# Performance work log

Measured on AMD Instinct MI355X. Metric: run time of the kernel, lower is better.

Reference implementation:

```python
import jax, jax.numpy as jnp
import numpy as np

DIM = 768
HEADS = 12
HD = DIM // HEADS  # 64
BASE = 100.0


def rope_sincos(H, W):
    # DINOv3 RopePositionEmbedding: normalize_coords='separate', base=100.0
    dd = HD // 4
    periods = BASE ** (jnp.arange(dd, dtype=jnp.float32) / dd)          # [dd]
    ch = (jnp.arange(H, dtype=jnp.float32) + 0.5) / H                    # pixel centers
    cw = (jnp.arange(W, dtype=jnp.float32) + 0.5) / W
    cy, cx = jnp.meshgrid(ch, cw, indexing='ij')
    coords = 2.0 * jnp.stack([cy, cx], axis=-1).reshape(H * W, 2) - 1.0  # [N,2] in [-1,1]
    angles = 2.0 * jnp.pi * coords[:, :, None] / periods[None, None, :]  # [N,2,dd]
    angles = angles.reshape(H * W, 2 * dd)                               # [N, HD//2]
    angles = jnp.concatenate([angles, angles], axis=-1)                  # [N, HD]
    return jnp.sin(angles), jnp.cos(angles)


def rotate_half(t):
    t1, t2 = jnp.split(t, 2, axis=-1)
    return jnp.concatenate([-t2, t1], axis=-1)


def setup_inputs() -> dict:
    key = jax.random.key(0)
    k1, k2, k3 = jax.random.split(key, 3)
    B, H, W = 2, 48, 48
    x = jax.random.normal(k1, (B, H, W, DIM), dtype=jnp.float32)
    w_qkv = jax.random.normal(k2, (3 * DIM, DIM), dtype=jnp.float32) * 0.02
    b_qkv = jnp.zeros((3 * DIM,), dtype=jnp.float32)
    w_proj = jax.random.normal(k3, (DIM, DIM), dtype=jnp.float32) * 0.02
    b_proj = jnp.zeros((DIM,), dtype=jnp.float32)
    return {"x": x, "w_qkv": w_qkv, "b_qkv": b_qkv, "w_proj": w_proj, "b_proj": b_proj}


def reference(x, w_qkv, b_qkv, w_proj, b_proj):
    B, H, W, C = x.shape
    N = H * W
    xf = x.reshape(B, N, C)
    qkv = xf @ w_qkv.T + b_qkv                                   # [B,N,3C]
    qkv = qkv.reshape(B, N, 3, HEADS, HD).transpose(2, 0, 3, 1, 4)
    q, k, v = qkv[0], qkv[1], qkv[2]                              # [B,h,N,d]
    sin, cos = rope_sincos(H, W)                                  # [N,d]
    q = q * cos + rotate_half(q) * sin
    k = k * cos + rotate_half(k) * sin
    scale = HD ** -0.5
    attn = jax.nn.softmax(jnp.einsum('bhqd,bhkd->bhqk', q, k) * scale, axis=-1)
    o = jnp.einsum('bhqk,bhkd->bhqd', attn, v)                    # [B,h,N,d]
    o = o.transpose(0, 2, 1, 3).reshape(B, N, C)
    o = o @ w_proj.T + b_proj
    return o.reshape(B, H, W, C)
```

## Files before the change

kernel.cpp:

```cpp
#include <hip/hip_runtime.h>

#define BATCH 2
#define NSEQ 2304
#define DIM 768
#define HEADS 12
#define HD 64
#define M_TOK (BATCH * NSEQ)
#define LDSP 72
#define KP 72

typedef __attribute__((ext_vector_type(8))) short bf16x8;
typedef __attribute__((ext_vector_type(4))) float f32x4;
typedef _Float16 half4 __attribute__((ext_vector_type(4)));

#define QSCALE (0.125f * 1.44269504088896f)

__device__ __forceinline__ short f2bf(float f) {
    union { float f; unsigned u; } v; v.f = f;
    unsigned r = v.u + 0x7fffu + ((v.u >> 16) & 1u);
    return (short)(r >> 16);
}
__device__ __forceinline__ float bf2f(short s) {
    union { unsigned u; float f; } v; v.u = ((unsigned)(unsigned short)s) << 16;
    return v.f;
}

__global__ void cvt_bf16_kernel(const float* __restrict__ in, short* __restrict__ out, int n4) {
    int i = blockIdx.x * 256 + threadIdx.x;
    if (i < n4) {
        float4 v = reinterpret_cast<const float4*>(in)[i];
        short4 o;
        o.x = f2bf(v.x); o.y = f2bf(v.y); o.z = f2bf(v.z); o.w = f2bf(v.w);
        reinterpret_cast<short4*>(out)[i] = o;
    }
}

__global__ __launch_bounds__(256) void gemm_qkv_kernel(
    const short* __restrict__ A,
    const short* __restrict__ Bt,
    const float* __restrict__ bias,
    short* __restrict__ qb, short* __restrict__ kbuf, _Float16* __restrict__ vtb)
{
    __shared__ __align__(16) short At[128 * LDSP];
    __shared__ __align__(16) short Bl[128 * LDSP];
    const int m0 = blockIdx.x * 128, n0 = blockIdx.y * 128;
    const int tid = threadIdx.x, lane = tid & 63, wave = tid >> 6;
    const int quad = lane >> 4, l16 = lane & 15;
    const int wm = (wave >> 1) * 64, wn = (wave & 1) * 64;
    const int r = tid >> 1, c0 = (tid & 1) * 32;
    f32x4 acc[4][4] = {};

    for (int k0 = 0; k0 < DIM; k0 += 64) {
        const uint4* ga = reinterpret_cast<const uint4*>(&A[(size_t)(m0 + r) * DIM + k0 + c0]);
        const uint4* gb = reinterpret_cast<const uint4*>(&Bt[(size_t)(n0 + r) * DIM + k0 + c0]);
        uint4 a0 = ga[0], a1 = ga[1], a2 = ga[2], a3 = ga[3];
        uint4 b0 = gb[0], b1 = gb[1], b2 = gb[2], b3 = gb[3];
        uint4* sa = reinterpret_cast<uint4*>(&At[r * LDSP + c0]);
        uint4* sb = reinterpret_cast<uint4*>(&Bl[r * LDSP + c0]);
        sa[0] = a0; sa[1] = a1; sa[2] = a2; sa[3] = a3;
        sb[0] = b0; sb[1] = b1; sb[2] = b2; sb[3] = b3;
        __syncthreads();
#pragma unroll
        for (int ks = 0; ks < 2; ++ks) {
            bf16x8 af[4], bf[4];
#pragma unroll
            for (int mt = 0; mt < 4; ++mt)
                af[mt] = *reinterpret_cast<const bf16x8*>(&At[(wm + mt * 16 + l16) * LDSP + ks * 32 + quad * 8]);
#pragma unroll
            for (int nt = 0; nt < 4; ++nt)
                bf[nt] = *reinterpret_cast<const bf16x8*>(&Bl[(wn + nt * 16 + l16) * LDSP + ks * 32 + quad * 8]);
#pragma unroll
            for (int mt = 0; mt < 4; ++mt)
#pragma unroll
                for (int nt = 0; nt < 4; ++nt)
                    acc[mt][nt] = __builtin_amdgcn_mfma_f32_16x16x32_bf16(af[mt], bf[nt], acc[mt][nt], 0, 0, 0);
        }
        __syncthreads();
    }

    const int which = (n0 + wn) / DIM;
    const int head = ((n0 + wn) % DIM) / HD;
    const int b = m0 / NSEQ;
    const int tokb = m0 % NSEQ + wm;
#pragma unroll
    for (int mt = 0; mt < 4; ++mt) {
#pragma unroll
        for (int nt = 0; nt < 4; ++nt) {
            const int n = n0 + wn + nt * 16 + l16;
            const int d = nt * 16 + l16;
            const float bi = bias[n];
            const int tok0 = tokb + mt * 16 + quad * 4;
            if (which == 2) {
                half4 hv;
                hv.x = (_Float16)(acc[mt][nt][0] + bi);
                hv.y = (_Float16)(acc[mt][nt][1] + bi);
                hv.z = (_Float16)(acc[mt][nt][2] + bi);
                hv.w = (_Float16)(acc[mt][nt][3] + bi);
                *reinterpret_cast<half4*>(&vtb[((size_t)(b * HEADS + head) * HD + d) * NSEQ + tok0]) = hv;
            } else {
                short* dst = (which == 0) ? qb : kbuf;
#pragma unroll
                for (int rg = 0; rg < 4; ++rg)
                    dst[((size_t)(b * HEADS + head) * NSEQ + tok0 + rg) * HD + d] =
                        f2bf(acc[mt][nt][rg] + bi);
            }
        }
    }
}

__global__ void rope_kernel(short* __restrict__ qb, short* __restrict__ kb) {
    int idx = blockIdx.x * 256 + threadIdx.x;
    if (idx >= BATCH * HEADS * NSEQ * 32) return;
    const int i = idx & 31;
    const int tok = (idx >> 5) % NSEQ;
    const int bh = idx / (32 * NSEQ);
    const int y = tok / 48, x = tok % 48;
    const int pi = (i < 16) ? i : (i - 16);
    const float coord = (i < 16) ? (2.0f * (y + 0.5f) / 48.0f - 1.0f)
                                 : (2.0f * (x + 0.5f) / 48.0f - 1.0f);
    const float period = powf(100.0f, (float)pi * (1.0f / 16.0f));
    const float ang = 2.0f * 3.14159265358979323846f * coord / period;
    const float s = sinf(ang), c = cosf(ang);
    const size_t base = ((size_t)bh * NSEQ + tok) * HD;
    float q1 = bf2f(qb[base + i]), q2 = bf2f(qb[base + i + 32]);
    qb[base + i]      = f2bf((q1 * c - q2 * s) * QSCALE);
    qb[base + i + 32] = f2bf((q2 * c + q1 * s) * QSCALE);
    float k1 = bf2f(kb[base + i]), k2 = bf2f(kb[base + i + 32]);
    kb[base + i]      = f2bf(k1 * c - k2 * s);
    kb[base + i + 32] = f2bf(k2 * c + k1 * s);
}

__global__ __launch_bounds__(256) void attn_kernel(
    const short* __restrict__ qb, const short* __restrict__ kb,
    const _Float16* __restrict__ vtb, short* __restrict__ ob)
{
    __shared__ __align__(16) short    Kt[2][64 * KP];
    __shared__ __align__(16) _Float16 Vt[2][64 * KP];
    const int qt = blockIdx.x, h = blockIdx.y, b = blockIdx.z;
    const int bh = b * HEADS + h;
    const int tid = threadIdx.x, lane = tid & 63, wave = tid >> 6;
    const int quad = lane >> 4, l16 = lane & 15;
    const int qrow0 = qt * 128 + wave * 32;
    const short* qbase = qb + (size_t)bh * NSEQ * HD;
    const short* kbase = kb + (size_t)bh * NSEQ * HD;
    const _Float16* vbase = vtb + (size_t)bh * HD * NSEQ;

    bf16x8 qf[2][2];
#pragma unroll
    for (int mt = 0; mt < 2; ++mt)
#pragma unroll
        for (int ks = 0; ks < 2; ++ks)
            qf[mt][ks] = *reinterpret_cast<const bf16x8*>(
                &qbase[(size_t)(qrow0 + mt * 16 + l16) * HD + ks * 32 + quad * 8]);

    half4 ones;
    ones.x = ones.y = ones.z = ones.w = (_Float16)1.0f;

    f32x4 oacc[2][4] = {};
    f32x4 lacc[2] = {};

    const int r = tid >> 2, cq = (tid & 3) * 16;
    {
        const uint4* gk = reinterpret_cast<const uint4*>(&kbase[(size_t)r * HD + cq]);
        uint4 k0 = gk[0], k1 = gk[1];
        const uint4* gv = reinterpret_cast<const uint4*>(&vbase[(size_t)r * NSEQ + cq]);
        uint4 v0 = gv[0], v1 = gv[1];
        uint4* sk = reinterpret_cast<uint4*>(&Kt[0][r * KP + cq]);
        sk[0] = k0; sk[1] = k1;
        uint4* sv = reinterpret_cast<uint4*>(&Vt[0][r * KP + cq]);
        sv[0] = v0; sv[1] = v1;
    }

    int cur = 0;
    const int NT = NSEQ / 64;
    for (int kt = 0; kt < NT; ++kt) {
        uint4 k0, k1, v0, v1;
        if (kt + 1 < NT) {
            const int nb0 = (kt + 1) * 64;
            const uint4* gk = reinterpret_cast<const uint4*>(&kbase[(size_t)(nb0 + r) * HD + cq]);
            k0 = gk[0]; k1 = gk[1];
            const uint4* gv = reinterpret_cast<const uint4*>(&vbase[(size_t)r * NSEQ + nb0 + cq]);
            v0 = gv[0]; v1 = gv[1];
        }
        __syncthreads();

        f32x4 sacc[4][2] = {};
#pragma unroll
        for (int ks = 0; ks < 2; ++ks) {
#pragma unroll
            for (int nt = 0; nt < 4; ++nt) {
                bf16x8 kf = *reinterpret_cast<const bf16x8*>(
                    &Kt[cur][(nt * 16 + l16) * KP + ks * 32 + quad * 8]);
#pragma unroll
                for (int mt = 0; mt < 2; ++mt)
                    sacc[nt][mt] = __builtin_amdgcn_mfma_f32_16x16x32_bf16(
                        kf, qf[mt][ks], sacc[nt][mt], 0, 0, 0);
            }
        }

        half4 pf[2][4];
#pragma unroll
        for (int mt = 0; mt < 2; ++mt)
#pragma unroll
            for (int nt = 0; nt < 4; ++nt) {
                pf[mt][nt].x = (_Float16)__builtin_amdgcn_exp2f(sacc[nt][mt][0]);
                pf[mt][nt].y = (_Float16)__builtin_amdgcn_exp2f(sacc[nt][mt][1]);
                pf[mt][nt].z = (_Float16)__builtin_amdgcn_exp2f(sacc[nt][mt][2]);
                pf[mt][nt].w = (_Float16)__builtin_amdgcn_exp2f(sacc[nt][mt][3]);
            }

#pragma unroll
        for (int mt = 0; mt < 2; ++mt)
#pragma unroll
            for (int nt = 0; nt < 4; ++nt)
                lacc[mt] = __builtin_amdgcn_mfma_f32_16x16x16f16(
                    pf[mt][nt], ones, lacc[mt], 0, 0, 0);

#pragma unroll
        for (int nt = 0; nt < 4; ++nt)
#pragma unroll
            for (int dt = 0; dt < 4; ++dt) {
                half4 vf = *reinterpret_cast<const half4*>(
                    &Vt[cur][(dt * 16 + l16) * KP + nt * 16 + quad * 4]);
#pragma unroll
                for (int mt = 0; mt < 2; ++mt)
                    oacc[mt][dt] = __builtin_amdgcn_mfma_f32_16x16x16f16(
                        pf[mt][nt], vf, oacc[mt][dt], 0, 0, 0);
            }

        if (kt + 1 < NT) {
            uint4* sk = reinterpret_cast<uint4*>(&Kt[cur ^ 1][r * KP + cq]);
            sk[0] = k0; sk[1] = k1;
            uint4* sv = reinterpret_cast<uint4*>(&Vt[cur ^ 1][r * KP + cq]);
            sv[0] = v0; sv[1] = v1;
        }
        cur ^= 1;
    }

#pragma unroll
    for (int mt = 0; mt < 2; ++mt) {
        float inv[4];
#pragma unroll
        for (int rg = 0; rg < 4; ++rg) inv[rg] = __builtin_amdgcn_rcpf(lacc[mt][rg]);
#pragma unroll
        for (int dt = 0; dt < 4; ++dt)
#pragma unroll
            for (int rg = 0; rg < 4; ++rg) {
                int row = qrow0 + mt * 16 + quad * 4 + rg;
                int col = h * HD + dt * 16 + l16;
                ob[((size_t)b * NSEQ + row) * DIM + col] = f2bf(oacc[mt][dt][rg] * inv[rg]);
            }
    }
}

__global__ __launch_bounds__(256) void gemm_proj_kernel(
    const short* __restrict__ A,
    const short* __restrict__ Bt,
    const float* __restrict__ bias,
    float* __restrict__ out)
{
    __shared__ __align__(16) short At[64 * LDSP];
    __shared__ __align__(16) short Bl[64 * LDSP];
    const int m0 = blockIdx.x * 64, n0 = blockIdx.y * 64;
    const int tid = threadIdx.x, lane = tid & 63, wave = tid >> 6;
    const int quad = lane >> 4, l16 = lane & 15;
    const int wm = (wave >> 1) * 32, wn = (wave & 1) * 32;
    const int r = tid >> 2, cs = (tid & 3) * 16;
    f32x4 acc[2][2] = {};

    for (int k0 = 0; k0 < DIM; k0 += 64) {
        const uint4* ga = reinterpret_cast<const uint4*>(&A[(size_t)(m0 + r) * DIM + k0 + cs]);
        uint4* sa = reinterpret_cast<uint4*>(&At[r * LDSP + cs]);
        sa[0] = ga[0]; sa[1] = ga[1];
        const uint4* gb = reinterpret_cast<const uint4*>(&Bt[(size_t)(n0 + r) * DIM + k0 + cs]);
        uint4* sb = reinterpret_cast<uint4*>(&Bl[r * LDSP + cs]);
        sb[0] = gb[0]; sb[1] = gb[1];
        __syncthreads();
#pragma unroll
        for (int ks = 0; ks < 2; ++ks) {
            bf16x8 af[2], bf[2];
#pragma unroll
            for (int mt = 0; mt < 2; ++mt)
                af[mt] = *reinterpret_cast<const bf16x8*>(&At[(wm + mt * 16 + l16) * LDSP + ks * 32 + quad * 8]);
#pragma unroll
            for (int nt = 0; nt < 2; ++nt)
                bf[nt] = *reinterpret_cast<const bf16x8*>(&Bl[(wn + nt * 16 + l16) * LDSP + ks * 32 + quad * 8]);
#pragma unroll
            for (int mt = 0; mt < 2; ++mt)
#pragma unroll
                for (int nt = 0; nt < 2; ++nt)
                    acc[mt][nt] = __builtin_amdgcn_mfma_f32_16x16x32_bf16(af[mt], bf[nt], acc[mt][nt], 0, 0, 0);
        }
        __syncthreads();
    }

#pragma unroll
    for (int mt = 0; mt < 2; ++mt)
#pragma unroll
        for (int nt = 0; nt < 2; ++nt) {
            const int n = n0 + wn + nt * 16 + l16;
            const float bi = bias[n];
#pragma unroll
            for (int rg = 0; rg < 4; ++rg) {
                const int m = m0 + wm + mt * 16 + quad * 4 + rg;
                out[(size_t)m * DIM + n] = acc[mt][nt][rg] + bi;
            }
        }
}

extern "C" void kernel_launch(void* const* d_in, const int* in_sizes, int n_in,
                              void* d_out, int out_size, void* d_ws, size_t ws_size,
                              hipStream_t stream) {
    const float* x      = (const float*)d_in[0];
    const float* w_qkv  = (const float*)d_in[1];
    const float* b_qkv  = (const float*)d_in[2];
    const float* w_proj = (const float*)d_in[3];
    const float* b_proj = (const float*)d_in[4];
    float* out = (float*)d_out;

    short* xb     = (short*)d_ws;
    short* wqkvb  = xb + (size_t)M_TOK * DIM;
    short* wprojb = wqkvb + (size_t)3 * DIM * DIM;
    short* qb     = wprojb + (size_t)DIM * DIM;
    short* kb     = qb + (size_t)BATCH * HEADS * NSEQ * HD;
    short* vtb    = kb + (size_t)BATCH * HEADS * NSEQ * HD;
    short* ob     = vtb + (size_t)BATCH * HEADS * NSEQ * HD;

    cvt_bf16_kernel<<<(M_TOK * DIM / 4 + 255) / 256, 256, 0, stream>>>(x, xb, M_TOK * DIM / 4);
    cvt_bf16_kernel<<<(3 * DIM * DIM / 4 + 255) / 256, 256, 0, stream>>>(w_qkv, wqkvb, 3 * DIM * DIM / 4);
    cvt_bf16_kernel<<<(DIM * DIM / 4 + 255) / 256, 256, 0, stream>>>(w_proj, wprojb, DIM * DIM / 4);

    dim3 g1(M_TOK / 128, 3 * DIM / 128);
    gemm_qkv_kernel<<<g1, 256, 0, stream>>>(xb, wqkvb, b_qkv, qb, kb, (_Float16*)vtb);

    int rope_n = BATCH * HEADS * NSEQ * 32;
    rope_kernel<<<(rope_n + 255) / 256, 256, 0, stream>>>(qb, kb);

    dim3 g2(NSEQ / 128, HEADS, BATCH);
    attn_kernel<<<g2, 256, 0, stream>>>(qb, kb, (const _Float16*)vtb, ob);

    dim3 g3(M_TOK / 64, DIM / 64);
    gemm_proj_kernel<<<g3, 256, 0, stream>>>(ob, wprojb, b_proj, out);
}
```

Baseline: 197.6 us.

## Split attention KV range in two, fuse RoPE into QKV epilogue and merge converts

```diff
diff --git a/kernel.cpp b/kernel.cpp
--- a/kernel.cpp
+++ b/kernel.cpp
@@ -8,12 +8,17 @@
 #define M_TOK (BATCH * NSEQ)
 #define LDSP 72
 #define KP 72
+#define BH (BATCH * HEADS)
+#define KT_HALF (NSEQ / 64 / 2)
 
 typedef __attribute__((ext_vector_type(8))) short bf16x8;
+typedef __attribute__((ext_vector_type(8))) short short8v;
 typedef __attribute__((ext_vector_type(4))) float f32x4;
 typedef _Float16 half4 __attribute__((ext_vector_type(4)));
+typedef _Float16 half8 __attribute__((ext_vector_type(8)));
 
 #define QSCALE (0.125f * 1.44269504088896f)
+#define LOG2_100_D16 0.41524101186092029f
 
 __device__ __forceinline__ short f2bf(float f) {
     union { float f; unsigned u; } v; v.f = f;
@@ -25,14 +30,22 @@
     return v.f;
 }
 
-__global__ void cvt_bf16_kernel(const float* __restrict__ in, short* __restrict__ out, int n4) {
+#define CN1 (M_TOK * DIM / 4)
+#define CN2 (3 * DIM * DIM / 4)
+#define CN3 (DIM * DIM / 4)
+__global__ void cvt_all_kernel(const float* __restrict__ x, const float* __restrict__ wq,
+                               const float* __restrict__ wp,
+                               short* __restrict__ xb, short* __restrict__ wqb,
+                               short* __restrict__ wpb) {
     int i = blockIdx.x * 256 + threadIdx.x;
-    if (i < n4) {
-        float4 v = reinterpret_cast<const float4*>(in)[i];
-        short4 o;
-        o.x = f2bf(v.x); o.y = f2bf(v.y); o.z = f2bf(v.z); o.w = f2bf(v.w);
-        reinterpret_cast<short4*>(out)[i] = o;
-    }
+    const float* src; short* dst; int j;
+    if (i < CN1)              { src = x;  dst = xb;  j = i; }
+    else if (i < CN1 + CN2)   { src = wq; dst = wqb; j = i - CN1; }
+    else                      { src = wp; dst = wpb; j = i - CN1 - CN2; }
+    float4 v = reinterpret_cast<const float4*>(src)[j];
+    short4 o;
+    o.x = f2bf(v.x); o.y = f2bf(v.y); o.z = f2bf(v.z); o.w = f2bf(v.w);
+    reinterpret_cast<short4*>(dst)[j] = o;
 }
 
 __global__ __launch_bounds__(256) void gemm_qkv_kernel(
@@ -82,62 +95,61 @@
     const int head = ((n0 + wn) % DIM) / HD;
     const int b = m0 / NSEQ;
     const int tokb = m0 % NSEQ + wm;
-#pragma unroll
-    for (int mt = 0; mt < 4; ++mt) {
-#pragma unroll
-        for (int nt = 0; nt < 4; ++nt) {
-            const int n = n0 + wn + nt * 16 + l16;
-            const int d = nt * 16 + l16;
-            const float bi = bias[n];
-            const int tok0 = tokb + mt * 16 + quad * 4;
-            if (which == 2) {
+    if (which == 2) {
+#pragma unroll
+        for (int mt = 0; mt < 4; ++mt)
+#pragma unroll
+            for (int nt = 0; nt < 4; ++nt) {
+                const int n = n0 + wn + nt * 16 + l16;
+                const int d = nt * 16 + l16;
+                const float bi = bias[n];
+                const int tok0 = tokb + mt * 16 + quad * 4;
                 half4 hv;
                 hv.x = (_Float16)(acc[mt][nt][0] + bi);
                 hv.y = (_Float16)(acc[mt][nt][1] + bi);
                 hv.z = (_Float16)(acc[mt][nt][2] + bi);
                 hv.w = (_Float16)(acc[mt][nt][3] + bi);
                 *reinterpret_cast<half4*>(&vtb[((size_t)(b * HEADS + head) * HD + d) * NSEQ + tok0]) = hv;
-            } else {
-                short* dst = (which == 0) ? qb : kbuf;
-#pragma unroll
-                for (int rg = 0; rg < 4; ++rg)
-                    dst[((size_t)(b * HEADS + head) * NSEQ + tok0 + rg) * HD + d] =
-                        f2bf(acc[mt][nt][rg] + bi);
-            }
-        }
-    }
-}
-
-__global__ void rope_kernel(short* __restrict__ qb, short* __restrict__ kb) {
-    int idx = blockIdx.x * 256 + threadIdx.x;
-    if (idx >= BATCH * HEADS * NSEQ * 32) return;
-    const int i = idx & 31;
-    const int tok = (idx >> 5) % NSEQ;
-    const int bh = idx / (32 * NSEQ);
-    const int y = tok / 48, x = tok % 48;
-    const int pi = (i < 16) ? i : (i - 16);
-    const float coord = (i < 16) ? (2.0f * (y + 0.5f) / 48.0f - 1.0f)
-                                 : (2.0f * (x + 0.5f) / 48.0f - 1.0f);
-    const float period = powf(100.0f, (float)pi * (1.0f / 16.0f));
-    const float ang = 2.0f * 3.14159265358979323846f * coord / period;
-    const float s = sinf(ang), c = cosf(ang);
-    const size_t base = ((size_t)bh * NSEQ + tok) * HD;
-    float q1 = bf2f(qb[base + i]), q2 = bf2f(qb[base + i + 32]);
-    qb[base + i]      = f2bf((q1 * c - q2 * s) * QSCALE);
-    qb[base + i + 32] = f2bf((q2 * c + q1 * s) * QSCALE);
-    float k1 = bf2f(kb[base + i]), k2 = bf2f(kb[base + i + 32]);
-    kb[base + i]      = f2bf(k1 * c - k2 * s);
-    kb[base + i + 32] = f2bf(k2 * c + k1 * s);
+            }
+    } else {
+        short* dst = (which == 0) ? qb : kbuf;
+        const float qs = (which == 0) ? QSCALE : 1.0f;
+        float bi[4];
+#pragma unroll
+        for (int nt = 0; nt < 4; ++nt) bi[nt] = bias[n0 + wn + nt * 16 + l16];
+        const float invp = __builtin_amdgcn_exp2f(-(float)l16 * LOG2_100_D16);
+#pragma unroll
+        for (int mt = 0; mt < 4; ++mt) {
+#pragma unroll
+            for (int rg = 0; rg < 4; ++rg) {
+                const int tok = tokb + mt * 16 + quad * 4 + rg;
+                const int yy = tok / 48, xx = tok - yy * 48;
+                const float ry = (2.0f * (yy + 0.5f) * (1.0f / 48.0f) - 1.0f) * invp;
+                const float rx = (2.0f * (xx + 0.5f) * (1.0f / 48.0f) - 1.0f) * invp;
+                const float sy = __builtin_amdgcn_sinf(ry), cy = __builtin_amdgcn_cosf(ry);
+                const float sx = __builtin_amdgcn_sinf(rx), cx = __builtin_amdgcn_cosf(rx);
+                const float a0 = acc[mt][0][rg] + bi[0];
+                const float a1 = acc[mt][1][rg] + bi[1];
+                const float a2 = acc[mt][2][rg] + bi[2];
+                const float a3 = acc[mt][3][rg] + bi[3];
+                short* rp = &dst[((size_t)(b * HEADS + head) * NSEQ + tok) * HD];
+                rp[l16]      = f2bf((a0 * cy - a2 * sy) * qs);
+                rp[32 + l16] = f2bf((a2 * cy + a0 * sy) * qs);
+                rp[16 + l16] = f2bf((a1 * cx - a3 * sx) * qs);
+                rp[48 + l16] = f2bf((a3 * cx + a1 * sx) * qs);
+            }
+        }
+    }
 }
 
 __global__ __launch_bounds__(256) void attn_kernel(
     const short* __restrict__ qb, const short* __restrict__ kb,
-    const _Float16* __restrict__ vtb, short* __restrict__ ob)
+    const _Float16* __restrict__ vtb, _Float16* __restrict__ opart,
+    float* __restrict__ lpart)
 {
     __shared__ __align__(16) short    Kt[2][64 * KP];
     __shared__ __align__(16) _Float16 Vt[2][64 * KP];
-    const int qt = blockIdx.x, h = blockIdx.y, b = blockIdx.z;
-    const int bh = b * HEADS + h;
+    const int qt = blockIdx.x, kh = blockIdx.y, bh = blockIdx.z;
     const int tid = threadIdx.x, lane = tid & 63, wave = tid >> 6;
     const int quad = lane >> 4, l16 = lane & 15;
     const int qrow0 = qt * 128 + wave * 32;
@@ -160,10 +172,11 @@
     f32x4 lacc[2] = {};
 
     const int r = tid >> 2, cq = (tid & 3) * 16;
+    const int t0 = kh * KT_HALF;
     {
-        const uint4* gk = reinterpret_cast<const uint4*>(&kbase[(size_t)r * HD + cq]);
+        const uint4* gk = reinterpret_cast<const uint4*>(&kbase[(size_t)(t0 * 64 + r) * HD + cq]);
         uint4 k0 = gk[0], k1 = gk[1];
-        const uint4* gv = reinterpret_cast<const uint4*>(&vbase[(size_t)r * NSEQ + cq]);
+        const uint4* gv = reinterpret_cast<const uint4*>(&vbase[(size_t)r * NSEQ + t0 * 64 + cq]);
         uint4 v0 = gv[0], v1 = gv[1];
         uint4* sk = reinterpret_cast<uint4*>(&Kt[0][r * KP + cq]);
         sk[0] = k0; sk[1] = k1;
@@ -172,11 +185,10 @@
     }
 
     int cur = 0;
-    const int NT = NSEQ / 64;
-    for (int kt = 0; kt < NT; ++kt) {
+    for (int kt = 0; kt < KT_HALF; ++kt) {
         uint4 k0, k1, v0, v1;
-        if (kt + 1 < NT) {
-            const int nb0 = (kt + 1) * 64;
+        if (kt + 1 < KT_HALF) {
+            const int nb0 = (t0 + kt + 1) * 64;
             const uint4* gk = reinterpret_cast<const uint4*>(&kbase[(size_t)(nb0 + r) * HD + cq]);
             k0 = gk[0]; k1 = gk[1];
             const uint4* gv = reinterpret_cast<const uint4*>(&vbase[(size_t)r * NSEQ + nb0 + cq]);
@@ -228,7 +240,7 @@
                         pf[mt][nt], vf, oacc[mt][dt], 0, 0, 0);
             }
 
-        if (kt + 1 < NT) {
+        if (kt + 1 < KT_HALF) {
             uint4* sk = reinterpret_cast<uint4*>(&Kt[cur ^ 1][r * KP + cq]);
             sk[0] = k0; sk[1] = k1;
             uint4* sv = reinterpret_cast<uint4*>(&Vt[cur ^ 1][r * KP + cq]);
@@ -237,24 +249,28 @@
         cur ^= 1;
     }
 
+    _Float16* ob2 = opart + (size_t)(kh * BH + bh) * NSEQ * HD;
+    float* lp2 = lpart + (size_t)(kh * BH + bh) * NSEQ;
 #pragma unroll
     for (int mt = 0; mt < 2; ++mt) {
-        float inv[4];
-#pragma unroll
-        for (int rg = 0; rg < 4; ++rg) inv[rg] = __builtin_amdgcn_rcpf(lacc[mt][rg]);
 #pragma unroll
         for (int dt = 0; dt < 4; ++dt)
 #pragma unroll
             for (int rg = 0; rg < 4; ++rg) {
                 int row = qrow0 + mt * 16 + quad * 4 + rg;
-                int col = h * HD + dt * 16 + l16;
-                ob[((size_t)b * NSEQ + row) * DIM + col] = f2bf(oacc[mt][dt][rg] * inv[rg]);
-            }
+                ob2[(size_t)row * HD + dt * 16 + l16] = (_Float16)oacc[mt][dt][rg];
+            }
+        if (l16 == 0) {
+#pragma unroll
+            for (int rg = 0; rg < 4; ++rg)
+                lp2[qrow0 + mt * 16 + quad * 4 + rg] = lacc[mt][rg];
+        }
     }
 }
 
 __global__ __launch_bounds__(256) void gemm_proj_kernel(
-    const short* __restrict__ A,
+    const _Float16* __restrict__ op,
+    const float* __restrict__ lp,
     const short* __restrict__ Bt,
     const float* __restrict__ bias,
     float* __restrict__ out)
@@ -266,15 +282,30 @@
     const int quad = lane >> 4, l16 = lane & 15;
     const int wm = (wave >> 1) * 32, wn = (wave & 1) * 32;
     const int r = tid >> 2, cs = (tid & 3) * 16;
+    const int b = m0 / NSEQ;
+    const int tok = m0 % NSEQ + r;
     f32x4 acc[2][2] = {};
 
     for (int k0 = 0; k0 < DIM; k0 += 64) {
-        const uint4* ga = reinterpret_cast<const uint4*>(&A[(size_t)(m0 + r) * DIM + k0 + cs]);
-        uint4* sa = reinterpret_cast<uint4*>(&At[r * LDSP + cs]);
-        sa[0] = ga[0]; sa[1] = ga[1];
+        const int h = k0 >> 6;
+        const size_t pb = (size_t)(b * HEADS + h) * NSEQ + tok;
+        const float l0 = lp[pb], l1 = lp[(size_t)BH * NSEQ + pb];
+        const float inv = __builtin_amdgcn_rcpf(l0 + l1);
+        const half8* o0 = reinterpret_cast<const half8*>(&op[pb * HD + cs]);
+        const half8* o1 = reinterpret_cast<const half8*>(&op[(size_t)BH * NSEQ * HD + pb * HD + cs]);
+        half8 p0 = o0[0], p1 = o0[1], q0 = o1[0], q1 = o1[1];
         const uint4* gb = reinterpret_cast<const uint4*>(&Bt[(size_t)(n0 + r) * DIM + k0 + cs]);
+        uint4 bw0 = gb[0], bw1 = gb[1];
+        short8v s0, s1;
+#pragma unroll
+        for (int j = 0; j < 8; ++j) {
+            s0[j] = f2bf(((float)p0[j] + (float)q0[j]) * inv);
+            s1[j] = f2bf(((float)p1[j] + (float)q1[j]) * inv);
+        }
+        *reinterpret_cast<short8v*>(&At[r * LDSP + cs]) = s0;
+        *reinterpret_cast<short8v*>(&At[r * LDSP + cs + 8]) = s1;
         uint4* sb = reinterpret_cast<uint4*>(&Bl[r * LDSP + cs]);
-        sb[0] = gb[0]; sb[1] = gb[1];
+        sb[0] = bw0; sb[1] = bw1;
         __syncthreads();
 #pragma unroll
         for (int ks = 0; ks < 2; ++ks) {
@@ -322,23 +353,22 @@
     short* wqkvb  = xb + (size_t)M_TOK * DIM;
     short* wprojb = wqkvb + (size_t)3 * DIM * DIM;
     short* qb     = wprojb + (size_t)DIM * DIM;
-    short* kb     = qb + (size_t)BATCH * HEADS * NSEQ * HD;
-    short* vtb    = kb + (size_t)BATCH * HEADS * NSEQ * HD;
-    short* ob     = vtb + (size_t)BATCH * HEADS * NSEQ * HD;
-
-    cvt_bf16_kernel<<<(M_TOK * DIM / 4 + 255) / 256, 256, 0, stream>>>(x, xb, M_TOK * DIM / 4);
-    cvt_bf16_kernel<<<(3 * DIM * DIM / 4 + 255) / 256, 256, 0, stream>>>(w_qkv, wqkvb, 3 * DIM * DIM / 4);
-    cvt_bf16_kernel<<<(DIM * DIM / 4 + 255) / 256, 256, 0, stream>>>(w_proj, wprojb, DIM * DIM / 4);
+    short* kb     = qb + (size_t)BH * NSEQ * HD;
+    short* vtb    = kb + (size_t)BH * NSEQ * HD;
+    short* opart  = vtb + (size_t)BH * NSEQ * HD;
+    float* lpart  = (float*)(opart + (size_t)2 * BH * NSEQ * HD);
+
+    cvt_all_kernel<<<(CN1 + CN2 + CN3) / 256, 256, 0, stream>>>(
+        x, w_qkv, w_proj, xb, wqkvb, wprojb);
 
     dim3 g1(M_TOK / 128, 3 * DIM / 128);
     gemm_qkv_kernel<<<g1, 256, 0, stream>>>(xb, wqkvb, b_qkv, qb, kb, (_Float16*)vtb);
 
-    int rope_n = BATCH * HEADS * NSEQ * 32;
-    rope_kernel<<<(rope_n + 255) / 256, 256, 0, stream>>>(qb, kb);
-
-    dim3 g2(NSEQ / 128, HEADS, BATCH);
-    attn_kernel<<<g2, 256, 0, stream>>>(qb, kb, (const _Float16*)vtb, ob);
+    dim3 g2(NSEQ / 128, 2, BH);
+    attn_kernel<<<g2, 256, 0, stream>>>(qb, kb, (const _Float16*)vtb,
+                                        (_Float16*)opart, lpart);
 
     dim3 g3(M_TOK / 64, DIM / 64);
-    gemm_proj_kernel<<<g3, 256, 0, stream>>>(ob, wprojb, b_proj, out);
-}
+    gemm_proj_kernel<<<g3, 256, 0, stream>>>((const _Float16*)opart, lpart,
+                                             wprojb, b_proj, out);
+}
```

Measured after the change: 184.9 us. 1.07x faster.
